# Performance work log

Measured on AMD Instinct MI355X. Metric: run time of the kernel, lower is better.

Reference implementation:

```python
import jax, jax.numpy as jnp
import numpy as np

N_NODES = 20000
N_EDGES = 320000
D_IN = 256
D_HID = 256
D_OUT = 128
N_LAYERS = 5
BN_EPS = 1e-5
W_SCALE = 1.0 / np.sqrt(D_HID)


def setup_inputs() -> dict:
    key = jax.random.key(0)
    ks = jax.random.split(key, 16)
    x = jax.random.normal(ks[0], (N_NODES, D_IN), dtype=jnp.float32)
    edge_index = jax.random.randint(ks[1], (2, N_EDGES), 0, N_NODES, dtype=jnp.int32)
    W1 = jax.random.normal(ks[2], (N_LAYERS, D_IN, D_HID), dtype=jnp.float32) * W_SCALE
    b1 = jax.random.normal(ks[3], (N_LAYERS, D_HID), dtype=jnp.float32) * 0.01
    W2a = jax.random.normal(ks[4], (N_LAYERS - 1, D_HID, D_HID), dtype=jnp.float32) * W_SCALE
    b2a = jax.random.normal(ks[5], (N_LAYERS - 1, D_HID), dtype=jnp.float32) * 0.01
    W2_last = jax.random.normal(ks[6], (D_HID, D_OUT), dtype=jnp.float32) * W_SCALE
    b2_last = jax.random.normal(ks[7], (D_OUT,), dtype=jnp.float32) * 0.01
    eps = jnp.zeros((N_LAYERS,), dtype=jnp.float32)
    bn_gamma = jnp.ones((N_LAYERS - 1, D_HID), dtype=jnp.float32)
    bn_beta = jnp.zeros((N_LAYERS - 1, D_HID), dtype=jnp.float32)
    bn_mean = jax.random.normal(ks[8], (N_LAYERS - 1, D_HID), dtype=jnp.float32) * 0.1
    bn_var = jax.random.uniform(ks[9], (N_LAYERS - 1, D_HID), dtype=jnp.float32, minval=0.5, maxval=1.5)
    return {"x": x, "edge_index": edge_index, "W1": W1, "b1": b1, "W2a": W2a,
            "b2a": b2a, "W2_last": W2_last, "b2_last": b2_last, "eps": eps,
            "bn_gamma": bn_gamma, "bn_beta": bn_beta, "bn_mean": bn_mean, "bn_var": bn_var}


def reference(x, edge_index, W1, b1, W2a, b2a, W2_last, b2_last, eps,
              bn_gamma, bn_beta, bn_mean, bn_var):
    src, dst = edge_index[0], edge_index[1]
    n = x.shape[0]

    def gin_conv(h, e, w1, bb1, w2, bb2):
        # scatter-add neighbor sum: agg[v] = sum_{(u->v)} h[u]
        agg = jax.ops.segment_sum(h[src], dst, num_segments=n)  # [N, d]
        z = (1.0 + e) * h + agg
        z = jax.nn.relu(z @ w1 + bb1)
        return z @ w2 + bb2

    h = x
    for i in range(N_LAYERS - 1):
        h = gin_conv(h, eps[i], W1[i], b1[i], W2a[i], b2a[i])
        # BatchNorm1d in eval mode (running stats); dropout inactive at inference
        h = (h - bn_mean[i]) * jax.lax.rsqrt(bn_var[i] + BN_EPS) * bn_gamma[i] + bn_beta[i]
        h = jax.nn.relu(h)
    out = gin_conv(h, eps[N_LAYERS - 1], W1[N_LAYERS - 1], b1[N_LAYERS - 1], W2_last, b2_last)
    return out
```

## Files before the change

### kernel.cpp

```cpp
#include <hip/hip_runtime.h>
#include <stdint.h>

#define NN    20000
#define NE    320000
#define MPAD  20096
#define NBLK  625
#define DD    256
#define DOUT  128
#define CAP   64
#define RS    40
#define SS    1288
#define STS   264
#define SFS   132

typedef unsigned short u16;
typedef unsigned char  u8;
typedef __attribute__((ext_vector_type(8))) __bf16 bf16x8;
typedef __attribute__((ext_vector_type(4))) float  f32x4;

__device__ __forceinline__ uint32_t f2b(float f){
  union { float f; uint32_t u; } x; x.f = f;
  uint32_t r = x.u + 0x7FFFu + ((x.u >> 16) & 1u);
  return r >> 16;
}
__device__ __forceinline__ float blo(uint32_t p){ union{uint32_t u;float f;}x; x.u=p<<16;         return x.f; }
__device__ __forceinline__ float bhi(uint32_t p){ union{uint32_t u;float f;}x; x.u=p&0xFFFF0000u; return x.f; }
__device__ __forceinline__ int   fiu(float f){ union{float f;int i;}x; x.f=f; return x.i; }
__device__ __forceinline__ float uif(int i){ union{int i;float f;}x; x.i=i; return x.f; }

__device__ __forceinline__ void acc4(float* a, uint32_t dw, float s){
  a[0] += s * (float)(int)(int8_t)(dw);
  a[1] += s * (float)(int)(int8_t)(dw >> 8);
  a[2] += s * (float)(int)(int8_t)(dw >> 16);
  a[3] += s * (float)(int)(int8_t)(dw >> 24);
}

#define TB 152
#define XB (MPAD/4)
#define EB ((NE+255)/256)
__global__ __launch_bounds__(256) void prep_all(
    const float* __restrict__ x, const int* __restrict__ src, const int* __restrict__ dst,
    const float* __restrict__ W1, const float* __restrict__ W2a, const float* __restrict__ W2l,
    u16* __restrict__ W1t, u16* __restrict__ W2at, u16* __restrict__ W2lt,
    u8* __restrict__ hq0, float* __restrict__ hs0, int* __restrict__ cnt, int* __restrict__ csr)
{
  __shared__ u16 Ts[64][65];
  int b = blockIdx.x, tid = threadIdx.x;
  if (b < TB){
    const float* srcp; u16* dstp; int ldS, k0, n0;
    if (b < 80){
      int layer = b >> 4, sub = b & 15;
      srcp = W1 + layer*65536; dstp = W1t + layer*65536; ldS = 256;
      k0 = (sub >> 2)*64; n0 = (sub & 3)*64;
    } else if (b < 144){
      int bb = b - 80; int layer = bb >> 4, sub = bb & 15;
      srcp = W2a + layer*65536; dstp = W2at + layer*65536; ldS = 256;
      k0 = (sub >> 2)*64; n0 = (sub & 3)*64;
    } else {
      int sub = b - 144;
      srcp = W2l; dstp = W2lt; ldS = 128;
      k0 = (sub >> 1)*64; n0 = (sub & 1)*64;
    }
    int c = tid & 63, r0 = tid >> 6;
    #pragma unroll
    for (int i = 0; i < 16; ++i){
      int r = r0 + i*4;
      Ts[r][c] = (u16)f2b(srcp[(size_t)(k0 + r)*ldS + n0 + c]);
    }
    __syncthreads();
    #pragma unroll
    for (int i = 0; i < 16; ++i){
      int n = r0 + i*4;
      dstp[(size_t)(n0 + n)*256 + k0 + c] = Ts[c][n];
    }
  } else if (b < TB + XB){
    int bb = b - TB;
    int row  = bb*4 + (tid >> 6);
    int lane = tid & 63;
    float4 f = make_float4(0.f,0.f,0.f,0.f);
    if (row < NN) f = *(const float4*)(x + (size_t)row*DD + lane*4);
    float mx = fmaxf(fmaxf(fabsf(f.x), fabsf(f.y)), fmaxf(fabsf(f.z), fabsf(f.w)));
    #pragma unroll
    for (int m = 1; m < 64; m <<= 1) mx = fmaxf(mx, __shfl_xor(mx, m, 64));
    float inv = mx > 0.f ? 127.0f/mx : 0.f;
    uint32_t pk = 0;
    pk |= (uint32_t)(u8)(int8_t)__float2int_rn(f.x*inv);
    pk |= (uint32_t)(u8)(int8_t)__float2int_rn(f.y*inv) << 8;
    pk |= (uint32_t)(u8)(int8_t)__float2int_rn(f.z*inv) << 16;
    pk |= (uint32_t)(u8)(int8_t)__float2int_rn(f.w*inv) << 24;
    if (row < MPAD){
      *(uint32_t*)(hq0 + (size_t)row*DD + lane*4) = pk;
      if (lane == 0) hs0[row] = mx * (1.0f/127.0f);
    }
  } else {
    int e = (b - TB - XB)*256 + tid;
    if (e < NE){
      int d = dst[e];
      int slot = atomicAdd(&cnt[d], 1);
      if (slot < CAP) csr[d*CAP + slot] = src[e];
    }
  }
}

__global__ __launch_bounds__(256, 3) void gin_fused(
    const u8* __restrict__ hq, const float* __restrict__ hs,
    const int* __restrict__ cnt, const int* __restrict__ csr,
    const float* __restrict__ eps_arr, int layer,
    const u16* __restrict__ w1, const float* __restrict__ b1,
    const u16* __restrict__ w2, const float* __restrict__ b2,
    const float* __restrict__ gma, const float* __restrict__ bta,
    const float* __restrict__ mu,  const float* __restrict__ var,
    u8* __restrict__ hqo, float* __restrict__ hso,
    float* __restrict__ outf, int last)
{
  __shared__ __align__(16) u16 As[8*SS];
  int tid  = threadIdx.x;
  int lane = tid & 63, w = tid >> 6;
  int m0 = blockIdx.x * 32;
  int l15 = lane & 15, l4 = lane >> 4;

  {
    float e = 1.0f + eps_arr[layer];
    int q2 = lane >> 4, kl = lane & 15;
    int x16 = (lane ^ 16) << 2;
    int x32 = (lane ^ 32) << 2;
    const u8* hrow = hq + kl*16;
    for (int i = 0; i < 8; ++i){
      int row = w*8 + i;
      int v = __builtin_amdgcn_readfirstlane(m0 + row);
      float a[16];
      #pragma unroll
      for (int j = 0; j < 16; ++j) a[j] = 0.f;
      int deg = cnt[v]; deg = deg > CAP ? CAP : deg;
      const int* lst = csr + (size_t)v*CAP;
      for (int base = 0; base < deg; base += 16){
        int4 qv[4];
        #pragma unroll
        for (int c = 0; c < 4; ++c) qv[c] = *(const int4*)(lst + base + 4*c);
        uint4 rv[4]; float sv[4];
        #pragma unroll
        for (int c = 0; c < 4; ++c){
          int slot = base + 4*c + q2;
          int eidx = q2 == 0 ? qv[c].x : q2 == 1 ? qv[c].y : q2 == 2 ? qv[c].z : qv[c].w;
          int g = slot < deg ? eidx : v;
          rv[c] = *(const uint4*)(hrow + (size_t)g*DD);
          float s = hs[g];
          sv[c] = slot < deg ? s : 0.f;
        }
        #pragma unroll
        for (int c = 0; c < 4; ++c){
          acc4(a +  0, rv[c].x, sv[c]);
          acc4(a +  4, rv[c].y, sv[c]);
          acc4(a +  8, rv[c].z, sv[c]);
          acc4(a + 12, rv[c].w, sv[c]);
        }
      }
      {
        uint4 ov = *(const uint4*)(hrow + (size_t)v*DD);
        float se = (q2 == 0) ? e * hs[v] : 0.f;
        acc4(a +  0, ov.x, se);
        acc4(a +  4, ov.y, se);
        acc4(a +  8, ov.z, se);
        acc4(a + 12, ov.w, se);
      }
      #pragma unroll
      for (int j = 0; j < 16; ++j){
        a[j] += uif(__builtin_amdgcn_ds_bpermute(x16, fiu(a[j])));
        a[j] += uif(__builtin_amdgcn_ds_bpermute(x32, fiu(a[j])));
      }
      if (q2 == 0){
        uint4 o1, o2;
        o1.x = f2b(a[0])  | (f2b(a[1])  << 16);
        o1.y = f2b(a[2])  | (f2b(a[3])  << 16);
        o1.z = f2b(a[4])  | (f2b(a[5])  << 16);
        o1.w = f2b(a[6])  | (f2b(a[7])  << 16);
        o2.x = f2b(a[8])  | (f2b(a[9])  << 16);
        o2.y = f2b(a[10]) | (f2b(a[11]) << 16);
        o2.z = f2b(a[12]) | (f2b(a[13]) << 16);
        o2.w = f2b(a[14]) | (f2b(a[15]) << 16);
        u16* dstL = As + (kl >> 1)*SS + row*RS + (kl & 1)*16;
        *(uint4*)(dstL)     = o1;
        *(uint4*)(dstL + 8) = o2;
      }
    }
  }
  __syncthreads();

  f32x4 acc1[4][2];
  #pragma unroll
  for (int i=0;i<4;++i)
    #pragma unroll
    for (int j=0;j<2;++j){ f32x4 zr={0.f,0.f,0.f,0.f}; acc1[i][j]=zr; }
  {
    int hidb = w*64;
    for (int s = 0; s < 8; ++s){
      bf16x8 af[4], bz[2];
      #pragma unroll
      for (int mi=0;mi<4;++mi)
        af[mi] = *(const bf16x8*)(w1 + (size_t)(hidb + mi*16 + l15)*DD + s*32 + l4*8);
      #pragma unroll
      for (int nj=0;nj<2;++nj)
        bz[nj] = *(const bf16x8*)(As + s*SS + (nj*16 + l15)*RS + l4*8);
      #pragma unroll
      for (int mi=0;mi<4;++mi)
        #pragma unroll
        for (int nj=0;nj<2;++nj)
          acc1[mi][nj] = __builtin_amdgcn_mfma_f32_16x16x32_bf16(af[mi], bz[nj], acc1[mi][nj], 0,0,0);
    }
  }
  __syncthreads();

  {
    int hidb = w*64;
    #pragma unroll
    for (int mi=0;mi<4;++mi){
      float4 bv = *(const float4*)(b1 + hidb + mi*16 + l4*4);
      int s2 = w*2 + (mi >> 1);
      int kp = (mi & 1)*16 + l4*4;
      #pragma unroll
      for (int nj=0;nj<2;++nj){
        int zrow = nj*16 + l15;
        float v0 = acc1[mi][nj][0] + bv.x; v0 = v0 > 0.f ? v0 : 0.f;
        float v1 = acc1[mi][nj][1] + bv.y; v1 = v1 > 0.f ? v1 : 0.f;
        float v2 = acc1[mi][nj][2] + bv.z; v2 = v2 > 0.f ? v2 : 0.f;
        float v3 = acc1[mi][nj][3] + bv.w; v3 = v3 > 0.f ? v3 : 0.f;
        uint2 pk;
        pk.x = f2b(v0) | (f2b(v1) << 16);
        pk.y = f2b(v2) | (f2b(v3) << 16);
        *(uint2*)(As + s2*SS + zrow*RS + kp) = pk;
      }
    }
  }
  __syncthreads();

  if (!last){
    f32x4 acc2[2][4];
    #pragma unroll
    for (int i=0;i<2;++i)
      #pragma unroll
      for (int j=0;j<4;++j){ f32x4 zr={0.f,0.f,0.f,0.f}; acc2[i][j]=zr; }
    int cb = w*64;
    for (int s = 0; s < 8; ++s){
      bf16x8 at[2], bw[4];
      #pragma unroll
      for (int i=0;i<2;++i)
        at[i] = *(const bf16x8*)(As + s*SS + (i*16 + l15)*RS + l4*8);
      #pragma unroll
      for (int j=0;j<4;++j)
        bw[j] = *(const bf16x8*)(w2 + (size_t)(cb + j*16 + l15)*DD + s*32 + l4*8);
      #pragma unroll
      for (int i=0;i<2;++i)
        #pragma unroll
        for (int j=0;j<4;++j)
          acc2[i][j] = __builtin_amdgcn_mfma_f32_16x16x32_bf16(at[i], bw[j], acc2[i][j], 0,0,0);
    }
    __syncthreads();
    u16* St = As;
    #pragma unroll
    for (int j=0;j<4;++j){
      int col = cb + j*16 + l15;
      float sc = rsqrtf(var[col] + 1e-5f) * gma[col];
      float sh = (b2[col] - mu[col]) * sc + bta[col];
      #pragma unroll
      for (int i=0;i<2;++i){
        #pragma unroll
        for (int r=0;r<4;++r){
          int row = i*16 + l4*4 + r;
          float vv = acc2[i][j][r]*sc + sh;
          vv = vv > 0.f ? vv : 0.f;
          St[row*STS + col] = (u16)f2b(vv);
        }
      }
    }
    __syncthreads();
    #pragma unroll
    for (int it = 0; it < 4; ++it){
      int idx = it*256 + tid;
      int row = idx >> 5, c = idx & 31;
      uint4 pk = *(const uint4*)(St + row*STS + c*8);
      float f0 = blo(pk.x), f1 = bhi(pk.x), f2 = blo(pk.y), f3 = bhi(pk.y);
      float f4 = blo(pk.z), f5 = bhi(pk.z), f6 = blo(pk.w), f7 = bhi(pk.w);
      float mx = fmaxf(fmaxf(fmaxf(f0,f1), fmaxf(f2,f3)), fmaxf(fmaxf(f4,f5), fmaxf(f6,f7)));
      #pragma unroll
      for (int m = 1; m < 32; m <<= 1) mx = fmaxf(mx, __shfl_xor(mx, m, 64));
      float inv = mx > 0.f ? 127.0f/mx : 0.f;
      uint32_t b0 = 0, b1v = 0;
      b0  |= (uint32_t)(u8)(int8_t)__float2int_rn(f0*inv);
      b0  |= (uint32_t)(u8)(int8_t)__float2int_rn(f1*inv) << 8;
      b0  |= (uint32_t)(u8)(int8_t)__float2int_rn(f2*inv) << 16;
      b0  |= (uint32_t)(u8)(int8_t)__float2int_rn(f3*inv) << 24;
      b1v |= (uint32_t)(u8)(int8_t)__float2int_rn(f4*inv);
      b1v |= (uint32_t)(u8)(int8_t)__float2int_rn(f5*inv) << 8;
      b1v |= (uint32_t)(u8)(int8_t)__float2int_rn(f6*inv) << 16;
      b1v |= (uint32_t)(u8)(int8_t)__float2int_rn(f7*inv) << 24;
      *(uint2*)(hqo + (size_t)(m0 + row)*DD + c*8) = make_uint2(b0, b1v);
      if (c == 0) hso[m0 + row] = mx * (1.0f/127.0f);
    }
  } else {
    f32x4 acc2[2][2];
    #pragma unroll
    for (int i=0;i<2;++i)
      #pragma unroll
      for (int j=0;j<2;++j){ f32x4 zr={0.f,0.f,0.f,0.f}; acc2[i][j]=zr; }
    int cbk = w*32;
    for (int s = 0; s < 8; ++s){
      bf16x8 at[2], bw[2];
      #pragma unroll
      for (int i=0;i<2;++i)
        at[i] = *(const bf16x8*)(As + s*SS + (i*16 + l15)*RS + l4*8);
      #pragma unroll
      for (int j=0;j<2;++j)
        bw[j] = *(const bf16x8*)(w2 + (size_t)(cbk + j*16 + l15)*DD + s*32 + l4*8);
      #pragma unroll
      for (int i=0;i<2;++i)
        #pragma unroll
        for (int j=0;j<2;++j)
          acc2[i][j] = __builtin_amdgcn_mfma_f32_16x16x32_bf16(at[i], bw[j], acc2[i][j], 0,0,0);
    }
    __syncthreads();
    float* Sf = (float*)As;
    #pragma unroll
    for (int j=0;j<2;++j){
      int col = cbk + j*16 + l15;
      float sh = b2[col];
      #pragma unroll
      for (int i=0;i<2;++i){
        #pragma unroll
        for (int r=0;r<4;++r){
          int row = i*16 + l4*4 + r;
          Sf[row*SFS + col] = acc2[i][j][r] + sh;
        }
      }
    }
    __syncthreads();
    #pragma unroll
    for (int it = 0; it < 4; ++it){
      int idx = it*256 + tid;
      int row = idx >> 5, c = idx & 31;
      *(uint4*)(outf + (size_t)(m0 + row)*DOUT + c*4) = *(const uint4*)(Sf + row*SFS + c*4);
    }
  }
}

extern "C" void kernel_launch(void* const* d_in, const int* in_sizes, int n_in,
                              void* d_out, int out_size, void* d_ws, size_t ws_size,
                              hipStream_t stream)
{
  const float* x     = (const float*)d_in[0];
  const int*   ei    = (const int*)  d_in[1];
  const float* W1    = (const float*)d_in[2];
  const float* b1    = (const float*)d_in[3];
  const float* W2a   = (const float*)d_in[4];
  const float* b2a   = (const float*)d_in[5];
  const float* W2l   = (const float*)d_in[6];
  const float* b2l   = (const float*)d_in[7];
  const float* eps   = (const float*)d_in[8];
  const float* gma   = (const float*)d_in[9];
  const float* bta   = (const float*)d_in[10];
  const float* mu    = (const float*)d_in[11];
  const float* var   = (const float*)d_in[12];
  float* out = (float*)d_out;

  char* ws = (char*)d_ws;
  size_t off = 0;
  auto alloc = [&](size_t bytes)->void*{
    void* p = ws + off; off += (bytes + 255) & ~(size_t)255; return p;
  };
  u8*    hq0 = (u8*)   alloc((size_t)MPAD*DD);
  u8*    hq1 = (u8*)   alloc((size_t)MPAD*DD);
  float* hs0 = (float*)alloc((size_t)MPAD*4);
  float* hs1 = (float*)alloc((size_t)MPAD*4);
  int*   cnt = (int*)  alloc((size_t)NN*4);
  int*   csr = (int*)  alloc((size_t)NN*CAP*4 + 64);
  u16*  W1t  = (u16*)  alloc((size_t)5*65536*2);
  u16*  W2at = (u16*)  alloc((size_t)4*65536*2);
  u16*  W2lt = (u16*)  alloc((size_t)32768*2);

  const int* srcA = ei;
  const int* dstA = ei + NE;

  hipMemsetAsync(cnt, 0, (size_t)NN*4, stream);
  prep_all<<<TB + XB + EB, 256, 0, stream>>>(x, srcA, dstA, W1, W2a, W2l,
                                             W1t, W2at, W2lt, hq0, hs0, cnt, csr);

  u8*    hq[2] = { hq0, hq1 };
  float* hsv[2] = { hs0, hs1 };
  for (int L = 0; L < 5; ++L){
    const u8*    hin = hq[L & 1];
    const float* hsi = hsv[L & 1];
    u8*    ho  = hq[1 - (L & 1)];
    float* hso = hsv[1 - (L & 1)];
    if (L < 4){
      gin_fused<<<NBLK, 256, 0, stream>>>(hin, hsi, cnt, csr, eps, L,
          W1t + (size_t)L*65536, b1 + L*256,
          W2at + (size_t)L*65536, b2a + L*256,
          gma + L*256, bta + L*256, mu + L*256, var + L*256,
          ho, hso, nullptr, 0);
    } else {
      gin_fused<<<NBLK, 256, 0, stream>>>(hin, hsi, cnt, csr, eps, L,
          W1t + (size_t)4*65536, b1 + 4*256,
          W2lt, b2l,
          nullptr, nullptr, nullptr, nullptr,
          nullptr, nullptr, out, 1);
    }
  }
}
```

Before: 352.2 us.

## Halve rows per block, use offset-binary int8 features, prefetch self rows

Each block now processes 16 node rows instead of 32, doubling the block count and raising the occupancy hint from 3 to 4 waves per SIMD, with smaller shared buffers. Quantized features are stored as unsigned offset-by-128 bytes, so dequantization is a mask-and-convert instead of a sign extend; the offset is removed afterwards by subtracting 128 times the summed scales. Degree, self row and self scale for the four rows per wave are loaded up front. The trade-off is that each block reuses the weight tiles over only 16 rows, so weight traffic per row doubles and MFMA work per block halves.

Result: slower. 395.7 us (+12.4%).

```diff
diff --git a/kernel.cpp b/kernel.cpp
--- a/kernel.cpp
+++ b/kernel.cpp
@@ -4,12 +4,13 @@
 #define NN    20000
 #define NE    320000
 #define MPAD  20096
-#define NBLK  625
+#define NBLK  1250
+#define MROW  16
 #define DD    256
 #define DOUT  128
 #define CAP   64
 #define RS    40
-#define SS    1288
+#define SS    648
 #define STS   264
 #define SFS   132
 
@@ -28,11 +29,11 @@
 __device__ __forceinline__ int   fiu(float f){ union{float f;int i;}x; x.f=f; return x.i; }
 __device__ __forceinline__ float uif(int i){ union{int i;float f;}x; x.i=i; return x.f; }
 
-__device__ __forceinline__ void acc4(float* a, uint32_t dw, float s){
-  a[0] += s * (float)(int)(int8_t)(dw);
-  a[1] += s * (float)(int)(int8_t)(dw >> 8);
-  a[2] += s * (float)(int)(int8_t)(dw >> 16);
-  a[3] += s * (float)(int)(int8_t)(dw >> 24);
+__device__ __forceinline__ void accu4(float* a, uint32_t dw, float s){
+  a[0] += s * (float)(dw & 0xffu);
+  a[1] += s * (float)((dw >> 8) & 0xffu);
+  a[2] += s * (float)((dw >> 16) & 0xffu);
+  a[3] += s * (float)(dw >> 24);
 }
 
 #define TB 152
@@ -84,10 +85,10 @@
     for (int m = 1; m < 64; m <<= 1) mx = fmaxf(mx, __shfl_xor(mx, m, 64));
     float inv = mx > 0.f ? 127.0f/mx : 0.f;
     uint32_t pk = 0;
-    pk |= (uint32_t)(u8)(int8_t)__float2int_rn(f.x*inv);
-    pk |= (uint32_t)(u8)(int8_t)__float2int_rn(f.y*inv) << 8;
-    pk |= (uint32_t)(u8)(int8_t)__float2int_rn(f.z*inv) << 16;
-    pk |= (uint32_t)(u8)(int8_t)__float2int_rn(f.w*inv) << 24;
+    pk |= (uint32_t)(u8)(__float2int_rn(f.x*inv) + 128);
+    pk |= (uint32_t)(u8)(__float2int_rn(f.y*inv) + 128) << 8;
+    pk |= (uint32_t)(u8)(__float2int_rn(f.z*inv) + 128) << 16;
+    pk |= (uint32_t)(u8)(__float2int_rn(f.w*inv) + 128) << 24;
     if (row < MPAD){
       *(uint32_t*)(hq0 + (size_t)row*DD + lane*4) = pk;
       if (lane == 0) hs0[row] = mx * (1.0f/127.0f);
@@ -102,7 +103,7 @@
   }
 }
 
-__global__ __launch_bounds__(256, 3) void gin_fused(
+__global__ __launch_bounds__(256, 4) void gin_fused(
     const u8* __restrict__ hq, const float* __restrict__ hs,
     const int* __restrict__ cnt, const int* __restrict__ csr,
     const float* __restrict__ eps_arr, int layer,
@@ -116,7 +117,7 @@
   __shared__ __align__(16) u16 As[8*SS];
   int tid  = threadIdx.x;
   int lane = tid & 63, w = tid >> 6;
-  int m0 = blockIdx.x * 32;
+  int m0 = blockIdx.x * MROW;
   int l15 = lane & 15, l4 = lane >> 4;
 
   {
@@ -125,13 +126,26 @@
     int x16 = (lane ^ 16) << 2;
     int x32 = (lane ^ 32) << 2;
     const u8* hrow = hq + kl*16;
-    for (int i = 0; i < 8; ++i){
-      int row = w*8 + i;
-      int v = __builtin_amdgcn_readfirstlane(m0 + row);
+
+    int   vv[4], dg[4];
+    uint4 ovv[4];
+    float svv[4];
+    #pragma unroll
+    for (int i = 0; i < 4; ++i){
+      vv[i] = __builtin_amdgcn_readfirstlane(m0 + w*4 + i);
+      dg[i] = cnt[vv[i]];
+      ovv[i] = *(const uint4*)(hrow + (size_t)vv[i]*DD);
+      svv[i] = hs[vv[i]];
+    }
+
+    for (int i = 0; i < 4; ++i){
+      int row = w*4 + i;
+      int v = vv[i];
       float a[16];
       #pragma unroll
       for (int j = 0; j < 16; ++j) a[j] = 0.f;
-      int deg = cnt[v]; deg = deg > CAP ? CAP : deg;
+      float ssum = 0.f;
+      int deg = dg[i]; deg = deg > CAP ? CAP : deg;
       const int* lst = csr + (size_t)v*CAP;
       for (int base = 0; base < deg; base += 16){
         int4 qv[4];
@@ -149,20 +163,23 @@
         }
         #pragma unroll
         for (int c = 0; c < 4; ++c){
-          acc4(a +  0, rv[c].x, sv[c]);
-          acc4(a +  4, rv[c].y, sv[c]);
-          acc4(a +  8, rv[c].z, sv[c]);
-          acc4(a + 12, rv[c].w, sv[c]);
+          ssum += sv[c];
+          accu4(a +  0, rv[c].x, sv[c]);
+          accu4(a +  4, rv[c].y, sv[c]);
+          accu4(a +  8, rv[c].z, sv[c]);
+          accu4(a + 12, rv[c].w, sv[c]);
         }
       }
       {
-        uint4 ov = *(const uint4*)(hrow + (size_t)v*DD);
-        float se = (q2 == 0) ? e * hs[v] : 0.f;
-        acc4(a +  0, ov.x, se);
-        acc4(a +  4, ov.y, se);
-        acc4(a +  8, ov.z, se);
-        acc4(a + 12, ov.w, se);
-      }
+        float se = (q2 == 0) ? e * svv[i] : 0.f;
+        ssum += se;
+        accu4(a +  0, ovv[i].x, se);
+        accu4(a +  4, ovv[i].y, se);
+        accu4(a +  8, ovv[i].z, se);
+        accu4(a + 12, ovv[i].w, se);
+      }
+      #pragma unroll
+      for (int j = 0; j < 16; ++j) a[j] -= 128.0f * ssum;
       #pragma unroll
       for (int j = 0; j < 16; ++j){
         a[j] += uif(__builtin_amdgcn_ds_bpermute(x16, fiu(a[j])));
@@ -186,26 +203,20 @@
   }
   __syncthreads();
 
-  f32x4 acc1[4][2];
+  f32x4 acc1[4];
   #pragma unroll
-  for (int i=0;i<4;++i)
-    #pragma unroll
-    for (int j=0;j<2;++j){ f32x4 zr={0.f,0.f,0.f,0.f}; acc1[i][j]=zr; }
+  for (int i=0;i<4;++i){ f32x4 zr={0.f,0.f,0.f,0.f}; acc1[i]=zr; }
   {
     int hidb = w*64;
     for (int s = 0; s < 8; ++s){
-      bf16x8 af[4], bz[2];
+      bf16x8 af[4], bz;
       #pragma unroll
       for (int mi=0;mi<4;++mi)
         af[mi] = *(const bf16x8*)(w1 + (size_t)(hidb + mi*16 + l15)*DD + s*32 + l4*8);
-      #pragma unroll
-      for (int nj=0;nj<2;++nj)
-        bz[nj] = *(const bf16x8*)(As + s*SS + (nj*16 + l15)*RS + l4*8);
+      bz = *(const bf16x8*)(As + s*SS + l15*RS + l4*8);
       #pragma unroll
       for (int mi=0;mi<4;++mi)
-        #pragma unroll
-        for (int nj=0;nj<2;++nj)
-          acc1[mi][nj] = __builtin_amdgcn_mfma_f32_16x16x32_bf16(af[mi], bz[nj], acc1[mi][nj], 0,0,0);
+        acc1[mi] = __builtin_amdgcn_mfma_f32_16x16x32_bf16(af[mi], bz, acc1[mi], 0,0,0);
     }
   }
   __syncthreads();
@@ -217,42 +228,33 @@
       float4 bv = *(const float4*)(b1 + hidb + mi*16 + l4*4);
       int s2 = w*2 + (mi >> 1);
       int kp = (mi & 1)*16 + l4*4;
-      #pragma unroll
-      for (int nj=0;nj<2;++nj){
-        int zrow = nj*16 + l15;
-        float v0 = acc1[mi][nj][0] + bv.x; v0 = v0 > 0.f ? v0 : 0.f;
-        float v1 = acc1[mi][nj][1] + bv.y; v1 = v1 > 0.f ? v1 : 0.f;
-        float v2 = acc1[mi][nj][2] + bv.z; v2 = v2 > 0.f ? v2 : 0.f;
-        float v3 = acc1[mi][nj][3] + bv.w; v3 = v3 > 0.f ? v3 : 0.f;
-        uint2 pk;
-        pk.x = f2b(v0) | (f2b(v1) << 16);
-        pk.y = f2b(v2) | (f2b(v3) << 16);
-        *(uint2*)(As + s2*SS + zrow*RS + kp) = pk;
-      }
+      int zrow = l15;
+      float v0 = acc1[mi][0] + bv.x; v0 = v0 > 0.f ? v0 : 0.f;
+      float v1 = acc1[mi][1] + bv.y; v1 = v1 > 0.f ? v1 : 0.f;
+      float v2 = acc1[mi][2] + bv.z; v2 = v2 > 0.f ? v2 : 0.f;
+      float v3 = acc1[mi][3] + bv.w; v3 = v3 > 0.f ? v3 : 0.f;
+      uint2 pk;
+      pk.x = f2b(v0) | (f2b(v1) << 16);
+      pk.y = f2b(v2) | (f2b(v3) << 16);
+      *(uint2*)(As + s2*SS + zrow*RS + kp) = pk;
     }
   }
   __syncthreads();
 
   if (!last){
-    f32x4 acc2[2][4];
-    #pragma unroll
-    for (int i=0;i<2;++i)
-      #pragma unroll
-      for (int j=0;j<4;++j){ f32x4 zr={0.f,0.f,0.f,0.f}; acc2[i][j]=zr; }
+    f32x4 acc2[4];
+    #pragma unroll
+    for (int j=0;j<4;++j){ f32x4 zr={0.f,0.f,0.f,0.f}; acc2[j]=zr; }
     int cb = w*64;
     for (int s = 0; s < 8; ++s){
-      bf16x8 at[2], bw[4];
-      #pragma unroll
-      for (int i=0;i<2;++i)
-        at[i] = *(const bf16x8*)(As + s*SS + (i*16 + l15)*RS + l4*8);
+      bf16x8 at, bw[4];
+      at = *(const bf16x8*)(As + s*SS + l15*RS + l4*8);
       #pragma unroll
       for (int j=0;j<4;++j)
         bw[j] = *(const bf16x8*)(w2 + (size_t)(cb + j*16 + l15)*DD + s*32 + l4*8);
       #pragma unroll
-      for (int i=0;i<2;++i)
-        #pragma unroll
-        for (int j=0;j<4;++j)
-          acc2[i][j] = __builtin_amdgcn_mfma_f32_16x16x32_bf16(at[i], bw[j], acc2[i][j], 0,0,0);
+      for (int j=0;j<4;++j)
+        acc2[j] = __builtin_amdgcn_mfma_f32_16x16x32_bf16(at, bw[j], acc2[j], 0,0,0);
     }
     __syncthreads();
     u16* St = As;
@@ -262,19 +264,16 @@
       float sc = rsqrtf(var[col] + 1e-5f) * gma[col];
       float sh = (b2[col] - mu[col]) * sc + bta[col];
       #pragma unroll
-      for (int i=0;i<2;++i){
-        #pragma unroll
-        for (int r=0;r<4;++r){
-          int row = i*16 + l4*4 + r;
-          float vv = acc2[i][j][r]*sc + sh;
-          vv = vv > 0.f ? vv : 0.f;
-          St[row*STS + col] = (u16)f2b(vv);
-        }
-      }
-    }
-    __syncthreads();
-    #pragma unroll
-    for (int it = 0; it < 4; ++it){
+      for (int r=0;r<4;++r){
+        int row = l4*4 + r;
+        float vv = acc2[j][r]*sc + sh;
+        vv = vv > 0.f ? vv : 0.f;
+        St[row*STS + col] = (u16)f2b(vv);
+      }
+    }
+    __syncthreads();
+    #pragma unroll
+    for (int it = 0; it < 2; ++it){
       int idx = it*256 + tid;
       int row = idx >> 5, c = idx & 31;
       uint4 pk = *(const uint4*)(St + row*STS + c*8);
@@ -285,37 +284,31 @@
       for (int m = 1; m < 32; m <<= 1) mx = fmaxf(mx, __shfl_xor(mx, m, 64));
       float inv = mx > 0.f ? 127.0f/mx : 0.f;
       uint32_t b0 = 0, b1v = 0;
-      b0  |= (uint32_t)(u8)(int8_t)__float2int_rn(f0*inv);
-      b0  |= (uint32_t)(u8)(int8_t)__float2int_rn(f1*inv) << 8;
-      b0  |= (uint32_t)(u8)(int8_t)__float2int_rn(f2*inv) << 16;
-      b0  |= (uint32_t)(u8)(int8_t)__float2int_rn(f3*inv) << 24;
-      b1v |= (uint32_t)(u8)(int8_t)__float2int_rn(f4*inv);
-      b1v |= (uint32_t)(u8)(int8_t)__float2int_rn(f5*inv) << 8;
-      b1v |= (uint32_t)(u8)(int8_t)__float2int_rn(f6*inv) << 16;
-      b1v |= (uint32_t)(u8)(int8_t)__float2int_rn(f7*inv) << 24;
+      b0  |= (uint32_t)(u8)(__float2int_rn(f0*inv) + 128);
+      b0  |= (uint32_t)(u8)(__float2int_rn(f1*inv) + 128) << 8;
+      b0  |= (uint32_t)(u8)(__float2int_rn(f2*inv) + 128) << 16;
+      b0  |= (uint32_t)(u8)(__float2int_rn(f3*inv) + 128) << 24;
+      b1v |= (uint32_t)(u8)(__float2int_rn(f4*inv) + 128);
+      b1v |= (uint32_t)(u8)(__float2int_rn(f5*inv) + 128) << 8;
+      b1v |= (uint32_t)(u8)(__float2int_rn(f6*inv) + 128) << 16;
+      b1v |= (uint32_t)(u8)(__float2int_rn(f7*inv) + 128) << 24;
       *(uint2*)(hqo + (size_t)(m0 + row)*DD + c*8) = make_uint2(b0, b1v);
       if (c == 0) hso[m0 + row] = mx * (1.0f/127.0f);
     }
   } else {
-    f32x4 acc2[2][2];
-    #pragma unroll
-    for (int i=0;i<2;++i)
-      #pragma unroll
-      for (int j=0;j<2;++j){ f32x4 zr={0.f,0.f,0.f,0.f}; acc2[i][j]=zr; }
+    f32x4 acc2[2];
+    #pragma unroll
+    for (int j=0;j<2;++j){ f32x4 zr={0.f,0.f,0.f,0.f}; acc2[j]=zr; }
     int cbk = w*32;
     for (int s = 0; s < 8; ++s){
-      bf16x8 at[2], bw[2];
-      #pragma unroll
-      for (int i=0;i<2;++i)
-        at[i] = *(const bf16x8*)(As + s*SS + (i*16 + l15)*RS + l4*8);
+      bf16x8 at, bw[2];
+      at = *(const bf16x8*)(As + s*SS + l15*RS + l4*8);
       #pragma unroll
       for (int j=0;j<2;++j)
         bw[j] = *(const bf16x8*)(w2 + (size_t)(cbk + j*16 + l15)*DD + s*32 + l4*8);
       #pragma unroll
-      for (int i=0;i<2;++i)
-        #pragma unroll
-        for (int j=0;j<2;++j)
-          acc2[i][j] = __builtin_amdgcn_mfma_f32_16x16x32_bf16(at[i], bw[j], acc2[i][j], 0,0,0);
+      for (int j=0;j<2;++j)
+        acc2[j] = __builtin_amdgcn_mfma_f32_16x16x32_bf16(at, bw[j], acc2[j], 0,0,0);
     }
     __syncthreads();
     float* Sf = (float*)As;
@@ -324,17 +317,14 @@
       int col = cbk + j*16 + l15;
       float sh = b2[col];
       #pragma unroll
-      for (int i=0;i<2;++i){
-        #pragma unroll
-        for (int r=0;r<4;++r){
-          int row = i*16 + l4*4 + r;
-          Sf[row*SFS + col] = acc2[i][j][r] + sh;
-        }
-      }
-    }
-    __syncthreads();
-    #pragma unroll
-    for (int it = 0; it < 4; ++it){
+      for (int r=0;r<4;++r){
+        int row = l4*4 + r;
+        Sf[row*SFS + col] = acc2[j][r] + sh;
+      }
+    }
+    __syncthreads();
+    #pragma unroll
+    for (int it = 0; it < 2; ++it){
       int idx = it*256 + tid;
       int row = idx >> 5, c = idx & 31;
       *(uint4*)(outf + (size_t)(m0 + row)*DOUT + c*4) = *(const uint4*)(Sf + row*SFS + c*4);
```

## Software-pipeline neighbor gathers with offset-binary int8 and interleaved CSR layout

Applied to the files above, without the earlier changes.

Restructures the aggregation phase so index loads and neighbor row gathers for the next destination rows are issued before the current row is consumed, with two register buffers in flight. Quantization switches to offset-binary (unsigned +128) so dequantization is a mask-and-convert, with a correction subtracting 128 times the scale sum afterward. The CSR slots are stored interleaved per lane group so each quarter-wave reads a contiguous int4 pair. The self term is folded into the first padding slot. The cost is higher register pressure, which could lower occupancy under the launch bounds of 3 blocks.

Measured after the change: 344.6 us. 2.2% less time.

```diff
diff --git a/kernel.cpp b/kernel.cpp
--- a/kernel.cpp
+++ b/kernel.cpp
@@ -5,6 +5,7 @@
 #define NE    320000
 #define MPAD  20096
 #define NBLK  625
+#define MROW  32
 #define DD    256
 #define DOUT  128
 #define CAP   64
@@ -28,11 +29,11 @@
 __device__ __forceinline__ int   fiu(float f){ union{float f;int i;}x; x.f=f; return x.i; }
 __device__ __forceinline__ float uif(int i){ union{int i;float f;}x; x.i=i; return x.f; }
 
-__device__ __forceinline__ void acc4(float* a, uint32_t dw, float s){
-  a[0] += s * (float)(int)(int8_t)(dw);
-  a[1] += s * (float)(int)(int8_t)(dw >> 8);
-  a[2] += s * (float)(int)(int8_t)(dw >> 16);
-  a[3] += s * (float)(int)(int8_t)(dw >> 24);
+__device__ __forceinline__ void accu4(float* a, uint32_t dw, float s){
+  a[0] += s * (float)(dw & 0xffu);
+  a[1] += s * (float)((dw >> 8) & 0xffu);
+  a[2] += s * (float)((dw >> 16) & 0xffu);
+  a[3] += s * (float)(dw >> 24);
 }
 
 #define TB 152
@@ -84,10 +85,10 @@
     for (int m = 1; m < 64; m <<= 1) mx = fmaxf(mx, __shfl_xor(mx, m, 64));
     float inv = mx > 0.f ? 127.0f/mx : 0.f;
     uint32_t pk = 0;
-    pk |= (uint32_t)(u8)(int8_t)__float2int_rn(f.x*inv);
-    pk |= (uint32_t)(u8)(int8_t)__float2int_rn(f.y*inv) << 8;
-    pk |= (uint32_t)(u8)(int8_t)__float2int_rn(f.z*inv) << 16;
-    pk |= (uint32_t)(u8)(int8_t)__float2int_rn(f.w*inv) << 24;
+    pk |= (uint32_t)(u8)(__float2int_rn(f.x*inv) + 128);
+    pk |= (uint32_t)(u8)(__float2int_rn(f.y*inv) + 128) << 8;
+    pk |= (uint32_t)(u8)(__float2int_rn(f.z*inv) + 128) << 16;
+    pk |= (uint32_t)(u8)(__float2int_rn(f.w*inv) + 128) << 24;
     if (row < MPAD){
       *(uint32_t*)(hq0 + (size_t)row*DD + lane*4) = pk;
       if (lane == 0) hs0[row] = mx * (1.0f/127.0f);
@@ -97,7 +98,7 @@
     if (e < NE){
       int d = dst[e];
       int slot = atomicAdd(&cnt[d], 1);
-      if (slot < CAP) csr[d*CAP + slot] = src[e];
+      if (slot < CAP) csr[d*CAP + ((slot & 3) << 4) + (slot >> 2)] = src[e];
     }
   }
 }
@@ -116,7 +117,7 @@
   __shared__ __align__(16) u16 As[8*SS];
   int tid  = threadIdx.x;
   int lane = tid & 63, w = tid >> 6;
-  int m0 = blockIdx.x * 32;
+  int m0 = blockIdx.x * MROW;
   int l15 = lane & 15, l4 = lane >> 4;
 
   {
@@ -125,44 +126,73 @@
     int x16 = (lane ^ 16) << 2;
     int x32 = (lane ^ 32) << 2;
     const u8* hrow = hq + kl*16;
-    for (int i = 0; i < 8; ++i){
-      int row = w*8 + i;
-      int v = __builtin_amdgcn_readfirstlane(m0 + row);
+
+    int4 qa0, qb0, qa1, qb1;
+    int  v0, d0, v1, d1;
+    uint4 rv0[8], rv1[8];
+    float sr0[8], sr1[8];
+    int  vk0, dk0, vk1, dk1;
+
+    auto ISSUE_IDX = [&](int i, int4& A, int4& B, int& vv, int& dd){
+      int v = __builtin_amdgcn_readfirstlane(m0 + w*8 + i);
+      vv = v; dd = cnt[v];
+      const int* cp = csr + (size_t)v*CAP + q2*16;
+      A = *(const int4*)(cp);
+      B = *(const int4*)(cp + 4);
+    };
+    auto ISSUE_ROWS = [&](const int4& A, const int4& B, int vv, int dd,
+                          uint4* RV, float* SR, int& vK, int& dK){
+      int deg = dd > CAP ? CAP : dd;
+      vK = vv; dK = deg;
+      #pragma unroll
+      for (int j = 0; j < 8; ++j){
+        int idx = j==0?A.x: j==1?A.y: j==2?A.z: j==3?A.w:
+                  j==4?B.x: j==5?B.y: j==6?B.z: B.w;
+        int slot = j*4 + q2;
+        int g = slot < deg ? idx : vv;
+        RV[j] = *(const uint4*)(hrow + (size_t)g*DD);
+        SR[j] = hs[g];
+      }
+    };
+    auto CONSUME = [&](const uint4* RV, const float* SR, int vv, int deg, int rowIdx){
       float a[16];
       #pragma unroll
       for (int j = 0; j < 16; ++j) a[j] = 0.f;
-      int deg = cnt[v]; deg = deg > CAP ? CAP : deg;
-      const int* lst = csr + (size_t)v*CAP;
-      for (int base = 0; base < deg; base += 16){
-        int4 qv[4];
-        #pragma unroll
-        for (int c = 0; c < 4; ++c) qv[c] = *(const int4*)(lst + base + 4*c);
-        uint4 rv[4]; float sv[4];
-        #pragma unroll
-        for (int c = 0; c < 4; ++c){
-          int slot = base + 4*c + q2;
-          int eidx = q2 == 0 ? qv[c].x : q2 == 1 ? qv[c].y : q2 == 2 ? qv[c].z : qv[c].w;
-          int g = slot < deg ? eidx : v;
-          rv[c] = *(const uint4*)(hrow + (size_t)g*DD);
-          float s = hs[g];
-          sv[c] = slot < deg ? s : 0.f;
+      float ssum = 0.f;
+      #pragma unroll
+      for (int j = 0; j < 8; ++j){
+        int slot = j*4 + q2;
+        float s = slot < deg ? SR[j] : (slot == deg ? e*SR[j] : 0.f);
+        ssum += s;
+        accu4(a+0, RV[j].x, s); accu4(a+4,  RV[j].y, s);
+        accu4(a+8, RV[j].z, s); accu4(a+12, RV[j].w, s);
+      }
+      if (deg >= 32){
+        const int* cp = csr + (size_t)vv*CAP + q2*16;
+        int4 C = *(const int4*)(cp + 8);
+        int4 D = *(const int4*)(cp + 12);
+        #pragma unroll
+        for (int j2 = 0; j2 < 8; ++j2){
+          int idx = j2==0?C.x: j2==1?C.y: j2==2?C.z: j2==3?C.w:
+                    j2==4?D.x: j2==5?D.y: j2==6?D.z: D.w;
+          int slot = (8+j2)*4 + q2;
+          int g = slot < deg ? idx : vv;
+          uint4 r = *(const uint4*)(hrow + (size_t)g*DD);
+          float sraw = hs[g];
+          float s = slot < deg ? sraw : (slot == deg ? e*sraw : 0.f);
+          ssum += s;
+          accu4(a+0, r.x, s); accu4(a+4,  r.y, s);
+          accu4(a+8, r.z, s); accu4(a+12, r.w, s);
         }
-        #pragma unroll
-        for (int c = 0; c < 4; ++c){
-          acc4(a +  0, rv[c].x, sv[c]);
-          acc4(a +  4, rv[c].y, sv[c]);
-          acc4(a +  8, rv[c].z, sv[c]);
-          acc4(a + 12, rv[c].w, sv[c]);
+        if (deg >= CAP){
+          uint4 ov = *(const uint4*)(hrow + (size_t)vv*DD);
+          float s = e * hs[vv]; ssum += s;
+          accu4(a+0, ov.x, s); accu4(a+4,  ov.y, s);
+          accu4(a+8, ov.z, s); accu4(a+12, ov.w, s);
         }
       }
-      {
-        uint4 ov = *(const uint4*)(hrow + (size_t)v*DD);
-        float se = (q2 == 0) ? e * hs[v] : 0.f;
-        acc4(a +  0, ov.x, se);
-        acc4(a +  4, ov.y, se);
-        acc4(a +  8, ov.z, se);
-        acc4(a + 12, ov.w, se);
-      }
+      #pragma unroll
+      for (int j = 0; j < 16; ++j) a[j] -= 128.0f * ssum;
       #pragma unroll
       for (int j = 0; j < 16; ++j){
         a[j] += uif(__builtin_amdgcn_ds_bpermute(x16, fiu(a[j])));
@@ -178,11 +208,36 @@
         o2.y = f2b(a[10]) | (f2b(a[11]) << 16);
         o2.z = f2b(a[12]) | (f2b(a[13]) << 16);
         o2.w = f2b(a[14]) | (f2b(a[15]) << 16);
-        u16* dstL = As + (kl >> 1)*SS + row*RS + (kl & 1)*16;
+        u16* dstL = As + (kl >> 1)*SS + rowIdx*RS + (kl & 1)*16;
         *(uint4*)(dstL)     = o1;
         *(uint4*)(dstL + 8) = o2;
       }
-    }
+    };
+
+    ISSUE_IDX(0, qa0, qb0, v0, d0);
+    ISSUE_IDX(1, qa1, qb1, v1, d1);
+    ISSUE_ROWS(qa0, qb0, v0, d0, rv0, sr0, vk0, dk0);
+    ISSUE_IDX(2, qa0, qb0, v0, d0);
+    ISSUE_ROWS(qa1, qb1, v1, d1, rv1, sr1, vk1, dk1);
+    ISSUE_IDX(3, qa1, qb1, v1, d1);
+    CONSUME(rv0, sr0, vk0, dk0, w*8 + 0);
+    ISSUE_ROWS(qa0, qb0, v0, d0, rv0, sr0, vk0, dk0);
+    ISSUE_IDX(4, qa0, qb0, v0, d0);
+    CONSUME(rv1, sr1, vk1, dk1, w*8 + 1);
+    ISSUE_ROWS(qa1, qb1, v1, d1, rv1, sr1, vk1, dk1);
+    ISSUE_IDX(5, qa1, qb1, v1, d1);
+    CONSUME(rv0, sr0, vk0, dk0, w*8 + 2);
+    ISSUE_ROWS(qa0, qb0, v0, d0, rv0, sr0, vk0, dk0);
+    ISSUE_IDX(6, qa0, qb0, v0, d0);
+    CONSUME(rv1, sr1, vk1, dk1, w*8 + 3);
+    ISSUE_ROWS(qa1, qb1, v1, d1, rv1, sr1, vk1, dk1);
+    ISSUE_IDX(7, qa1, qb1, v1, d1);
+    CONSUME(rv0, sr0, vk0, dk0, w*8 + 4);
+    ISSUE_ROWS(qa0, qb0, v0, d0, rv0, sr0, vk0, dk0);
+    CONSUME(rv1, sr1, vk1, dk1, w*8 + 5);
+    ISSUE_ROWS(qa1, qb1, v1, d1, rv1, sr1, vk1, dk1);
+    CONSUME(rv0, sr0, vk0, dk0, w*8 + 6);
+    CONSUME(rv1, sr1, vk1, dk1, w*8 + 7);
   }
   __syncthreads();
 
@@ -285,14 +340,14 @@
       for (int m = 1; m < 32; m <<= 1) mx = fmaxf(mx, __shfl_xor(mx, m, 64));
       float inv = mx > 0.f ? 127.0f/mx : 0.f;
       uint32_t b0 = 0, b1v = 0;
-      b0  |= (uint32_t)(u8)(int8_t)__float2int_rn(f0*inv);
-      b0  |= (uint32_t)(u8)(int8_t)__float2int_rn(f1*inv) << 8;
-      b0  |= (uint32_t)(u8)(int8_t)__float2int_rn(f2*inv) << 16;
-      b0  |= (uint32_t)(u8)(int8_t)__float2int_rn(f3*inv) << 24;
-      b1v |= (uint32_t)(u8)(int8_t)__float2int_rn(f4*inv);
-      b1v |= (uint32_t)(u8)(int8_t)__float2int_rn(f5*inv) << 8;
-      b1v |= (uint32_t)(u8)(int8_t)__float2int_rn(f6*inv) << 16;
-      b1v |= (uint32_t)(u8)(int8_t)__float2int_rn(f7*inv) << 24;
+      b0  |= (uint32_t)(u8)(__float2int_rn(f0*inv) + 128);
+      b0  |= (uint32_t)(u8)(__float2int_rn(f1*inv) + 128) << 8;
+      b0  |= (uint32_t)(u8)(__float2int_rn(f2*inv) + 128) << 16;
+      b0  |= (uint32_t)(u8)(__float2int_rn(f3*inv) + 128) << 24;
+      b1v |= (uint32_t)(u8)(__float2int_rn(f4*inv) + 128);
+      b1v |= (uint32_t)(u8)(__float2int_rn(f5*inv) + 128) << 8;
+      b1v |= (uint32_t)(u8)(__float2int_rn(f6*inv) + 128) << 16;
+      b1v |= (uint32_t)(u8)(__float2int_rn(f7*inv) + 128) << 24;
       *(uint2*)(hqo + (size_t)(m0 + row)*DD + c*8) = make_uint2(b0, b1v);
       if (c == 0) hso[m0 + row] = mx * (1.0f/127.0f);
     }
```
